# Kernel tuning notes

Measured on AMD Instinct MI355X. Metric: run time of the kernel, lower is better.

Reference implementation:

```python
import jax, jax.numpy as jnp
import numpy as np

B, T, C = 2, 2048, 1024
H = 16
HD = C // H  # head_size = 64
FF = 4 * C
EPS = 1e-5


def layernorm(x, g, b):
    mu = jnp.mean(x, axis=-1, keepdims=True)
    var = jnp.mean(jnp.square(x - mu), axis=-1, keepdims=True)
    return (x - mu) * jax.lax.rsqrt(var + EPS) * g + b


def setup_inputs() -> dict:
    key = jax.random.key(0)
    ks = jax.random.split(key, 12)
    s_c = 1.0 / np.sqrt(C)
    s_hc = 1.0 / np.sqrt(C)
    s_ff = 1.0 / np.sqrt(FF)
    return {
        "x": jax.random.normal(ks[0], (B, T, C), jnp.float32),
        "Wq": jax.random.normal(ks[1], (H, C, HD), jnp.float32) * s_hc,
        "Wk": jax.random.normal(ks[2], (H, C, HD), jnp.float32) * s_hc,
        "Wv": jax.random.normal(ks[3], (H, C, HD), jnp.float32) * s_hc,
        "Wo": jax.random.normal(ks[4], (C, C), jnp.float32) * s_c,
        "bo": jax.random.normal(ks[5], (C,), jnp.float32) * 0.01,
        "W1": jax.random.normal(ks[6], (C, FF), jnp.float32) * s_c,
        "b1": jax.random.normal(ks[7], (FF,), jnp.float32) * 0.01,
        "W2": jax.random.normal(ks[8], (FF, C), jnp.float32) * s_ff,
        "b2": jax.random.normal(ks[9], (C,), jnp.float32) * 0.01,
        "g1": jnp.ones((C,), jnp.float32),
        "be1": jnp.zeros((C,), jnp.float32),
        "g2": jnp.ones((C,), jnp.float32),
        "be2": jnp.zeros((C,), jnp.float32),
    }


def reference(x, Wq, Wk, Wv, Wo, bo, W1, b1, W2, b2, g1, be1, g2, be2):
    # --- self-attention sublayer (pre-LN, residual) ---
    h = layernorm(x, g1, be1)                               # [B,T,C]
    q = jnp.einsum("btc,hcd->bhtd", h, Wq)                   # [B,H,T,HD]
    k = jnp.einsum("btc,hcd->bhtd", h, Wk)
    v = jnp.einsum("btc,hcd->bhtd", h, Wv)
    scores = jnp.einsum("bhtd,bhsd->bhts", q, k) * (HD ** -0.5)
    causal = jnp.tril(jnp.ones((T, T), bool))
    scores = jnp.where(causal, scores, -jnp.inf)
    wei = jax.nn.softmax(scores, axis=-1)                    # [B,H,T,T]
    attn = jnp.einsum("bhts,bhsd->bhtd", wei, v)             # [B,H,T,HD]
    attn = attn.transpose(0, 2, 1, 3).reshape(B, T, H * HD)  # concat heads
    x = x + attn @ Wo + bo
    # --- feedforward sublayer (pre-LN, residual) ---
    h2 = layernorm(x, g2, be2)
    x = x + jax.nn.relu(h2 @ W1 + b1) @ W2 + b2
    return x
```

## Files before the change

### kernel.cpp

```cpp
#include <hip/hip_runtime.h>
#include <hip/hip_bf16.h>
#include <cstdint>
#include <cstddef>
#include <cstring>

#define B_ 2
#define T_ 2048
#define C_ 1024
#define H_ 16
#define HD_ 64
#define FF_ 4096
#define BT_ (B_*T_)

typedef __attribute__((ext_vector_type(8))) short short8;
typedef __attribute__((ext_vector_type(4))) float f32x4;

__device__ __forceinline__ float bf2f(ushort u) {
    return __uint_as_float(((uint)u) << 16);
}
__device__ __forceinline__ ushort f2bf(float f) {
    uint x = __float_as_uint(f);
    return (ushort)((x + 0x7fffu + ((x >> 16) & 1u)) >> 16);
}
__device__ __forceinline__ ushort f2bf_hw(float f) {
    __hip_bfloat16 h = __float2bfloat16(f);
    ushort u;
    __builtin_memcpy(&u, &h, 2);
    return u;
}

#define GLDS16(g, l)                                                        \
    __builtin_amdgcn_global_load_lds(                                       \
        (const __attribute__((address_space(1))) void*)(g),                 \
        (__attribute__((address_space(3))) void*)(l), 16, 0, 0)

__global__ __launch_bounds__(256) void ln_kernel(const float* __restrict__ x,
                                                 const float* __restrict__ g,
                                                 const float* __restrict__ b,
                                                 ushort* __restrict__ out) {
    int row = blockIdx.x;
    int tid = threadIdx.x;
    const float* xr = x + (size_t)row * C_;
    float4 v = *(const float4*)(xr + tid * 4);
    float s = v.x + v.y + v.z + v.w;
    float q = v.x*v.x + v.y*v.y + v.z*v.z + v.w*v.w;
    #pragma unroll
    for (int off = 32; off > 0; off >>= 1) {
        s += __shfl_down(s, off);
        q += __shfl_down(q, off);
    }
    __shared__ float ss[4], qs[4];
    if ((tid & 63) == 0) { ss[tid >> 6] = s; qs[tid >> 6] = q; }
    __syncthreads();
    s = ss[0] + ss[1] + ss[2] + ss[3];
    q = qs[0] + qs[1] + qs[2] + qs[3];
    float mu  = s * (1.0f / C_);
    float var = q * (1.0f / C_) - mu * mu;
    float r = rsqrtf(var + 1e-5f);
    float4 gv = *(const float4*)(g + tid * 4);
    float4 bv = *(const float4*)(b + tid * 4);
    ushort4 o;
    o.x = f2bf((v.x - mu) * r * gv.x + bv.x);
    o.y = f2bf((v.y - mu) * r * gv.y + bv.y);
    o.z = f2bf((v.z - mu) * r * gv.z + bv.z);
    o.w = f2bf((v.w - mu) * r * gv.w + bv.w);
    *(ushort4*)(out + (size_t)row * C_ + tid * 4) = o;
}

__global__ __launch_bounds__(256) void tcvt_kernel(const float* __restrict__ in,
                                                   ushort* __restrict__ out,
                                                   int R, int Cc, int ldo,
                                                   long in_bs, long out_bs) {
    __shared__ float tile[32][33];
    const float* inz = in + (size_t)blockIdx.z * in_bs;
    ushort* outz = out + (size_t)blockIdx.z * out_bs;
    int c0 = blockIdx.x * 32, r0 = blockIdx.y * 32;
    #pragma unroll
    for (int i = 0; i < 4; i++) {
        int r = threadIdx.y + i * 8;
        tile[r][threadIdx.x] = inz[(size_t)(r0 + r) * Cc + c0 + threadIdx.x];
    }
    __syncthreads();
    #pragma unroll
    for (int i = 0; i < 4; i++) {
        int c = threadIdx.y + i * 8;
        outz[(size_t)(c0 + c) * ldo + r0 + threadIdx.x] = f2bf(tile[threadIdx.x][c]);
    }
}

template<int EPI, bool OUT_BF16>
__global__ __launch_bounds__(512, 4) void gemm2(
    const ushort* __restrict__ A,
    const ushort* __restrict__ Bt,
    void* __restrict__ Cout,
    const float* __restrict__ bias,
    const float* __restrict__ resid,
    int M, int N, int K, int KS)
{
    __shared__ ushort As[2][128 * 32];
    __shared__ ushort Bs[2][256 * 32];

    int gx = gridDim.x;
    int nwg = gx * gridDim.y;
    int bid = blockIdx.y * gx + blockIdx.x;
    int cpx = nwg >> 3;
    int swz = (bid & 7) * cpx + (bid >> 3);
    int bx = swz % gx, by = swz / gx;

    int tid  = threadIdx.x;
    int lane = tid & 63;
    int lr = lane & 15, lq = lane >> 4;
    int wave = tid >> 6;
    int wr = wave >> 2, wc = wave & 3;
    int m0 = by * 128, n0 = bx * 256;
    int Koff = blockIdx.z * KS;
    size_t zoff = (size_t)blockIdx.z * ((size_t)M * N);

    f32x4 acc[4][4];
    #pragma unroll
    for (int i = 0; i < 4; i++)
        #pragma unroll
        for (int j = 0; j < 4; j++)
            acc[i][j] = {0.f, 0.f, 0.f, 0.f};

    int srow = tid >> 2;
    int scol = ((tid & 3) ^ ((srow >> 1) & 3)) * 8;
    const ushort* gA  = A  + (size_t)(m0 + srow) * K + Koff + scol;
    const ushort* gB0 = Bt + (size_t)(n0 + srow) * K + Koff + scol;
    const ushort* gB1 = Bt + (size_t)(n0 + 128 + srow) * K + Koff + scol;
    int NT = KS / 32;

    auto stage = [&](int kt, int buf) {
        int off = kt * 32;
        GLDS16(gA + off,  (char*)As[buf] + wave * 1024);
        GLDS16(gB0 + off, (char*)Bs[buf] + wave * 1024);
        GLDS16(gB1 + off, (char*)Bs[buf] + 8192 + wave * 1024);
    };

    stage(0, 0);
    stage(1, 1);
    asm volatile("s_waitcnt vmcnt(3)" ::: "memory");
    __builtin_amdgcn_s_barrier();

    int so = (lq ^ ((lr >> 1) & 3)) << 4;

    int cur = 0;
    for (int t = 0; t < NT; ++t) {
        const char* Ab = (const char*)As[cur] + (wr * 64 + lr) * 64 + so;
        const char* Bb = (const char*)Bs[cur] + (wc * 64 + lr) * 64 + so;

        short8 a[4], b[4];
        #pragma unroll
        for (int fr = 0; fr < 4; fr++)
            a[fr] = *(const short8*)(Ab + fr * 1024);
        #pragma unroll
        for (int fc = 0; fc < 4; fc++)
            b[fc] = *(const short8*)(Bb + fc * 1024);
        asm volatile("s_waitcnt lgkmcnt(0)" ::: "memory");
        __builtin_amdgcn_sched_barrier(0);
        __builtin_amdgcn_s_barrier();

        if (t + 2 < NT) stage(t + 2, cur);

        __builtin_amdgcn_s_setprio(1);
        #pragma unroll
        for (int fr = 0; fr < 4; fr++)
            #pragma unroll
            for (int fc = 0; fc < 4; fc++)
                acc[fr][fc] = __builtin_amdgcn_mfma_f32_16x16x32_bf16(
                    a[fr], b[fc], acc[fr][fc], 0, 0, 0);
        __builtin_amdgcn_s_setprio(0);

        if (t + 1 == NT) break;
        if (t + 2 < NT)
            asm volatile("s_waitcnt vmcnt(3)" ::: "memory");
        else
            asm volatile("s_waitcnt vmcnt(0)" ::: "memory");
        __builtin_amdgcn_s_barrier();
        cur ^= 1;
    }

    #pragma unroll
    for (int fr = 0; fr < 4; fr++) {
        #pragma unroll
        for (int fc = 0; fc < 4; fc++) {
            int col = n0 + wc * 64 + fc * 16 + lr;
            #pragma unroll
            for (int j = 0; j < 4; j++) {
                int row = m0 + wr * 64 + fr * 16 + lq * 4 + j;
                float v = acc[fr][fc][j];
                if (EPI & 1) v += bias[col];
                if (EPI & 2) v = fmaxf(v, 0.f);
                if (EPI & 4) v += resid[(size_t)row * N + col];
                if (OUT_BF16)
                    ((ushort*)Cout)[zoff + (size_t)row * N + col] = f2bf(v);
                else
                    ((float*)Cout)[zoff + (size_t)row * N + col] = v;
            }
        }
    }
}

__global__ __launch_bounds__(256) void vt_red(ushort* __restrict__ vt,
                                              const ushort* __restrict__ p) {
    size_t i = (size_t)blockIdx.x * 256 + threadIdx.x;
    ushort4 a = ((const ushort4*)p)[i];
    ushort4 b = ((const ushort4*)(p + (size_t)1024 * BT_))[i];
    ushort4 o;
    o.x = f2bf(bf2f(a.x) + bf2f(b.x));
    o.y = f2bf(bf2f(a.y) + bf2f(b.y));
    o.z = f2bf(bf2f(a.z) + bf2f(b.z));
    o.w = f2bf(bf2f(a.w) + bf2f(b.w));
    ((ushort4*)vt)[i] = o;
}

__global__ __launch_bounds__(256) void wo_ln(float* __restrict__ out,
                                             ushort* __restrict__ h,
                                             const ushort* __restrict__ p,
                                             const float* __restrict__ bo,
                                             const float* __restrict__ x,
                                             const float* __restrict__ g,
                                             const float* __restrict__ be) {
    int row = blockIdx.x;
    int tid = threadIdx.x;
    size_t base = (size_t)row * C_ + tid * 4;
    float4 v = *(const float4*)(x + base);
    float4 c = *(const float4*)(bo + tid * 4);
    #pragma unroll
    for (int z = 0; z < 4; z++) {
        ushort4 a = *(const ushort4*)(p + (size_t)z * BT_ * C_ + base);
        v.x += bf2f(a.x); v.y += bf2f(a.y);
        v.z += bf2f(a.z); v.w += bf2f(a.w);
    }
    v.x += c.x; v.y += c.y; v.z += c.z; v.w += c.w;
    *(float4*)(out + base) = v;

    float s = v.x + v.y + v.z + v.w;
    float q = v.x*v.x + v.y*v.y + v.z*v.z + v.w*v.w;
    #pragma unroll
    for (int off = 32; off > 0; off >>= 1) {
        s += __shfl_down(s, off);
        q += __shfl_down(q, off);
    }
    __shared__ float ss[4], qs[4];
    if ((tid & 63) == 0) { ss[tid >> 6] = s; qs[tid >> 6] = q; }
    __syncthreads();
    s = ss[0] + ss[1] + ss[2] + ss[3];
    q = qs[0] + qs[1] + qs[2] + qs[3];
    float mu  = s * (1.0f / C_);
    float var = q * (1.0f / C_) - mu * mu;
    float r = rsqrtf(var + 1e-5f);
    float4 gv = *(const float4*)(g + tid * 4);
    float4 bv = *(const float4*)(be + tid * 4);
    ushort4 o;
    o.x = f2bf((v.x - mu) * r * gv.x + bv.x);
    o.y = f2bf((v.y - mu) * r * gv.y + bv.y);
    o.z = f2bf((v.z - mu) * r * gv.z + bv.z);
    o.w = f2bf((v.w - mu) * r * gv.w + bv.w);
    *(ushort4*)(h + base) = o;
}

__global__ __launch_bounds__(256) void ff2_red4(float* __restrict__ out,
                                                const ushort* __restrict__ p,
                                                const float* __restrict__ b2) {
    size_t i = (size_t)blockIdx.x * 256 + threadIdx.x;
    float4 o = ((float4*)out)[i];
    float4 c = ((const float4*)b2)[i & 255];
    #pragma unroll
    for (int z = 0; z < 4; z++) {
        ushort4 a = ((const ushort4*)(p + (size_t)z * BT_ * C_))[i];
        o.x += bf2f(a.x); o.y += bf2f(a.y);
        o.z += bf2f(a.z); o.w += bf2f(a.w);
    }
    o.x += c.x; o.y += c.y; o.z += c.z; o.w += c.w;
    ((float4*)out)[i] = o;
}

__global__ __launch_bounds__(256, 3) void attn_mfma(const ushort* __restrict__ qk,
                                                    const ushort* __restrict__ vt,
                                                    ushort* __restrict__ Opart,
                                                    float* __restrict__ ml) {
    const float C2 = 0.18033688011f;
    const float THR2 = 12.0f;

    int flat = blockIdx.x;
    int xcd = flat & 7;
    int idx = flat >> 3;
    int bh  = xcd * 4 + (idx & 3);
    int qz  = idx >> 2;
    int qa  = 15 - (qz >> 1);
    int z   = qz & 1;

    int bb = bh >> 4;
    int head = bh & 15;
    int q0 = qa * 128;

    int tid  = threadIdx.x;
    int lane = tid & 63;
    int lr = lane & 15, lq = lane >> 4;
    int wave = tid >> 6;
    int qw = q0 + wave * 32;

    __shared__ ushort Ks[2][64 * 64];
    __shared__ ushort Vs[2][64 * 64];
    __shared__ ushort Ps[4][32 * 64];
    char* pw = (char*)Ps[wave];

    short8 qf[2][2];
    {
        const ushort* qb = qk + ((size_t)(bb * T_ + qw)) * 2048 + head * 64;
        #pragma unroll
        for (int mt = 0; mt < 2; mt++)
            #pragma unroll
            for (int kk = 0; kk < 2; kk++)
                qf[mt][kk] = *(const short8*)(qb + (size_t)(mt*16 + lr) * 2048 + kk*32 + lq*8);
    }

    f32x4 acc[2][4];
    f32x4 lsum[2];
    float m2[2][4];
    #pragma unroll
    for (int mt = 0; mt < 2; mt++) {
        #pragma unroll
        for (int dt = 0; dt < 4; dt++) acc[mt][dt] = {0.f, 0.f, 0.f, 0.f};
        lsum[mt] = {0.f, 0.f, 0.f, 0.f};
        #pragma unroll
        for (int j = 0; j < 4; j++) m2[mt][j] = -INFINITY;
    }

    const short8 onesf = {(short)0x3F80, (short)0x3F80, (short)0x3F80, (short)0x3F80,
                          (short)0x3F80, (short)0x3F80, (short)0x3F80, (short)0x3F80};

    int srow = tid >> 3;
    int ssc = ((tid & 7) ^ (srow & 7)) * 8;
    const ushort* kg0 = qk + ((size_t)(bb * T_ + srow)) * 2048 + 1024 + head * 64 + ssc;
    const ushort* vg0 = vt + ((size_t)(head * 64 + srow)) * 4096 + (size_t)bb * 2048 + ssc;

    auto stage = [&](int it, int buf) {
        int s0 = it * 64;
        char* Kb = (char*)Ks[buf] + wave * 1024;
        char* Vb = (char*)Vs[buf] + wave * 1024;
        GLDS16(kg0 + (size_t)s0 * 2048,        Kb);
        GLDS16(kg0 + (size_t)(s0 + 32) * 2048, Kb + 4096);
        GLDS16(vg0 + s0,                        Vb);
        GLDS16(vg0 + (size_t)32 * 4096 + s0,    Vb + 4096);
    };

    int nt = 2 * (qa + 1);
    stage(z, 0);
    __syncthreads();
    int cur = 0;

    for (int it = z; it < nt; it += 2) {
        if (it + 2 < nt) stage(it + 2, cur ^ 1);

        int s0h = it * 64;
        if (s0h <= qw + 31) {
            const ushort* Kc = Ks[cur];
            const ushort* Vc = Vs[cur];

            f32x4 sa[2][4];
            __builtin_amdgcn_s_setprio(1);
            #pragma unroll
            for (int n = 0; n < 4; n++) {
                int row = n*16 + lr;
                const char* kbase = (const char*)Kc + row*128;
                short8 kf0 = *(const short8*)(kbase + ((lq       ^ (row & 7)) << 4));
                short8 kf1 = *(const short8*)(kbase + (((4 + lq) ^ (row & 7)) << 4));
                #pragma unroll
                for (int mt = 0; mt < 2; mt++) {
                    f32x4 tq = {0.f, 0.f, 0.f, 0.f};
                    tq = __builtin_amdgcn_mfma_f32_16x16x32_bf16(qf[mt][0], kf0, tq, 0, 0, 0);
                    tq = __builtin_amdgcn_mfma_f32_16x16x32_bf16(qf[mt][1], kf1, tq, 0, 0, 0);
                    sa[mt][n] = tq;
                }
            }
            __builtin_amdgcn_s_setprio(0);

            if (s0h + 63 > qw) {
                #pragma unroll
                for (int mt = 0; mt < 2; mt++)
                    #pragma unroll
                    for (int n = 0; n < 4; n++)
                        #pragma unroll
                        for (int j = 0; j < 4; j++) {
                            int scolm = s0h + n*16 + lr;
                            int qrow = qw + mt*16 + lq*4 + j;
                            if (scolm > qrow) sa[mt][n][j] = -INFINITY;
                        }
            }

            float vmax2[2][4];
            bool growf = false;
            #pragma unroll
            for (int mt = 0; mt < 2; mt++) {
                #pragma unroll
                for (int j = 0; j < 4; j++) {
                    float v = fmaxf(fmaxf(sa[mt][0][j], sa[mt][1][j]),
                                    fmaxf(sa[mt][2][j], sa[mt][3][j]));
                    #pragma unroll
                    for (int off = 1; off < 16; off <<= 1)
                        v = fmaxf(v, __shfl_xor(v, off));
                    float v2 = v * C2;
                    vmax2[mt][j] = v2;
                    growf |= (v2 > m2[mt][j] + THR2);
                }
            }
            if (__any(growf)) {
                #pragma unroll
                for (int mt = 0; mt < 2; mt++)
                    #pragma unroll
                    for (int j = 0; j < 4; j++) {
                        float m2n = fmaxf(m2[mt][j], vmax2[mt][j]);
                        float corr = __builtin_amdgcn_exp2f(m2[mt][j] - m2n);
                        m2[mt][j] = m2n;
                        lsum[mt][j] *= corr;
                        #pragma unroll
                        for (int dt = 0; dt < 4; dt++)
                            acc[mt][dt][j] *= corr;
                    }
            }

            #pragma unroll
            for (int mt = 0; mt < 2; mt++)
                #pragma unroll
                for (int n = 0; n < 4; n++)
                    #pragma unroll
                    for (int j = 0; j < 4; j++) {
                        float p = __builtin_amdgcn_exp2f(
                            fmaf(sa[mt][n][j], C2, -m2[mt][j]));
                        int row = mt*16 + lq*4 + j;
                        int col = n*16 + lr;
                        int byte = row*128 + ((((col >> 3) ^ (row & 7))) << 4) + (col & 7)*2;
                        *(ushort*)(pw + byte) = f2bf_hw(p);
                    }

            short8 pf[2][2];
            #pragma unroll
            for (int mt = 0; mt < 2; mt++) {
                int row = mt*16 + lr;
                #pragma unroll
                for (int kk = 0; kk < 2; kk++)
                    pf[mt][kk] = *(const short8*)(pw + row*128
                                   + (((kk*4 + lq) ^ (row & 7)) << 4));
            }
            __builtin_amdgcn_s_setprio(1);
            #pragma unroll
            for (int kk = 0; kk < 2; kk++)
                #pragma unroll
                for (int mt = 0; mt < 2; mt++)
                    lsum[mt] = __builtin_amdgcn_mfma_f32_16x16x32_bf16(
                        pf[mt][kk], onesf, lsum[mt], 0, 0, 0);
            #pragma unroll
            for (int dt = 0; dt < 4; dt++) {
                int row = dt*16 + lr;
                const char* vbase = (const char*)Vc + row*128;
                #pragma unroll
                for (int kk = 0; kk < 2; kk++) {
                    short8 vf = *(const short8*)(vbase
                                  + (((kk*4 + lq) ^ (row & 7)) << 4));
                    #pragma unroll
                    for (int mt = 0; mt < 2; mt++)
                        acc[mt][dt] = __builtin_amdgcn_mfma_f32_16x16x32_bf16(
                            pf[mt][kk], vf, acc[mt][dt], 0, 0, 0);
                }
            }
            __builtin_amdgcn_s_setprio(0);
        }

        __syncthreads();
        cur ^= 1;
    }

    ushort* ob = Opart + (size_t)z * ((size_t)BT_ * C_)
               + ((size_t)(bb * T_ + qw)) * 1024 + head * 64;
    #pragma unroll
    for (int mt = 0; mt < 2; mt++)
        #pragma unroll
        for (int j = 0; j < 4; j++) {
            float l = lsum[mt][j];
            float inv = l > 0.f ? 1.0f / l : 0.f;
            #pragma unroll
            for (int dt = 0; dt < 4; dt++)
                ob[(size_t)(mt*16 + lq*4 + j) * 1024 + dt*16 + lr] =
                    f2bf(acc[mt][dt][j] * inv);
        }
    if (lr == 0) {
        float* mlz = ml + ((size_t)(z * 16 + head)) * (BT_ * 2);
        #pragma unroll
        for (int mt = 0; mt < 2; mt++)
            #pragma unroll
            for (int j = 0; j < 4; j++) {
                size_t row = (size_t)(bb * T_ + qw + mt*16 + lq*4 + j);
                *(float2*)(mlz + row * 2) = make_float2(m2[mt][j], lsum[mt][j]);
            }
    }
}

__global__ __launch_bounds__(256) void attn_comb(const ushort* __restrict__ Opart,
                                                 const float* __restrict__ ml,
                                                 ushort* __restrict__ outb) {
    int row = blockIdx.x;
    int tid = threadIdx.x;
    int col = tid * 4;
    int head = col >> 6;
    float2 ml0 = *(const float2*)(ml + ((size_t)head * BT_ + row) * 2);
    float2 ml1 = *(const float2*)(ml + ((size_t)(16 + head) * BT_ + row) * 2);
    float m = fmaxf(ml0.x, ml1.x);
    float w0 = ml0.y * __builtin_amdgcn_exp2f(ml0.x - m);
    float w1 = ml1.y * __builtin_amdgcn_exp2f(ml1.x - m);
    float inv = 1.0f / (w0 + w1);
    w0 *= inv; w1 *= inv;
    size_t idx = (size_t)row * C_ + col;
    ushort4 a = *(const ushort4*)(Opart + idx);
    ushort4 b = *(const ushort4*)(Opart + (size_t)BT_ * C_ + idx);
    ushort4 o;
    o.x = f2bf(bf2f(a.x) * w0 + bf2f(b.x) * w1);
    o.y = f2bf(bf2f(a.y) * w0 + bf2f(b.y) * w1);
    o.z = f2bf(bf2f(a.z) * w0 + bf2f(b.z) * w1);
    o.w = f2bf(bf2f(a.w) * w0 + bf2f(b.w) * w1);
    *(ushort4*)(outb + idx) = o;
}

extern "C" void kernel_launch(void* const* d_in, const int* in_sizes, int n_in,
                              void* d_out, int out_size, void* d_ws, size_t ws_size,
                              hipStream_t stream) {
    const float* x   = (const float*)d_in[0];
    const float* Wq  = (const float*)d_in[1];
    const float* Wk  = (const float*)d_in[2];
    const float* Wv  = (const float*)d_in[3];
    const float* Wo  = (const float*)d_in[4];
    const float* bo  = (const float*)d_in[5];
    const float* W1  = (const float*)d_in[6];
    const float* b1  = (const float*)d_in[7];
    const float* W2  = (const float*)d_in[8];
    const float* b2  = (const float*)d_in[9];
    const float* g1  = (const float*)d_in[10];
    const float* be1 = (const float*)d_in[11];
    const float* g2  = (const float*)d_in[12];
    const float* be2 = (const float*)d_in[13];
    float* out = (float*)d_out;

    char* ws = (char*)d_ws;
    const size_t MB = 1 << 20;
    ushort* h_bf    = (ushort*)(ws);
    ushort* qk_act  = (ushort*)(ws + 8*MB);
    ushort* vt      = (ushort*)(ws + 24*MB);
    ushort* attn_bf = (ushort*)(ws);
    ushort* W2_t    = (ushort*)(ws + 40*MB);
    ushort* qkvw    = (ushort*)(ws + 48*MB);
    ushort* Wo_t    = (ushort*)(ws + 54*MB);
    ushort* W1_t    = (ushort*)(ws + 56*MB);
    ushort* p_vt    = (ushort*)(ws + 64*MB);
    ushort* Opart   = (ushort*)(ws + 64*MB);
    float*  mlbuf   = (float*)(ws + 80*MB);
    ushort* p_wo    = (ushort*)(ws + 8*MB);
    ushort* ff1     = (ushort*)(ws + 8*MB);
    ushort* p_ff2   = (ushort*)(ws + 48*MB);

    const float* Wsrc[3] = {Wq, Wk, Wv};
    for (int w = 0; w < 3; w++) {
        tcvt_kernel<<<dim3(2, 32, 16), dim3(32, 8), 0, stream>>>(
            Wsrc[w], qkvw + (size_t)w * 1024 * 1024,
            1024, 64, 1024, 65536L, 65536L);
    }
    tcvt_kernel<<<dim3(32, 32, 1), dim3(32, 8), 0, stream>>>(
        Wo, Wo_t, 1024, 1024, 1024, 0L, 0L);
    tcvt_kernel<<<dim3(128, 32, 1), dim3(32, 8), 0, stream>>>(
        W1, W1_t, 1024, 4096, 1024, 0L, 0L);
    tcvt_kernel<<<dim3(32, 128, 1), dim3(32, 8), 0, stream>>>(
        W2, W2_t, 4096, 1024, 4096, 0L, 0L);

    ln_kernel<<<dim3(BT_), dim3(256), 0, stream>>>(x, g1, be1, h_bf);

    gemm2<0, true><<<dim3(2048/256, BT_/128, 1), dim3(512), 0, stream>>>(
        h_bf, qkvw, qk_act, nullptr, nullptr, BT_, 2048, C_, C_);
    gemm2<0, true><<<dim3(BT_/256, 1024/128, 2), dim3(512), 0, stream>>>(
        qkvw + (size_t)2*1024*1024, h_bf, p_vt, nullptr, nullptr, 1024, BT_, C_, 512);
    vt_red<<<dim3(1024*BT_/4/256), dim3(256), 0, stream>>>(vt, p_vt);

    attn_mfma<<<dim3(1024), dim3(256), 0, stream>>>(qk_act, vt, Opart, mlbuf);
    attn_comb<<<dim3(BT_), dim3(256), 0, stream>>>(Opart, mlbuf, attn_bf);

    gemm2<0, true><<<dim3(1024/256, BT_/128, 4), dim3(512), 0, stream>>>(
        attn_bf, Wo_t, p_wo, nullptr, nullptr, BT_, C_, C_, 256);
    wo_ln<<<dim3(BT_), dim3(256), 0, stream>>>(out, h_bf, p_wo, bo, x, g2, be2);

    gemm2<1|2, true><<<dim3(FF_/256, BT_/128, 1), dim3(512), 0, stream>>>(
        h_bf, W1_t, ff1, b1, nullptr, BT_, FF_, C_, C_);

    gemm2<0, true><<<dim3(1024/256, BT_/128, 4), dim3(512), 0, stream>>>(
        ff1, W2_t, p_ff2, nullptr, nullptr, BT_, C_, FF_, 1024);
    ff2_red4<<<dim3(BT_*C_/4/256), dim3(256), 0, stream>>>(out, p_ff2, b2);
}
```

Before: 259.3 us.

## Drop split-KV attention and combine pass; merge QKV weight conversions into one launch

```diff
diff --git a/kernel.cpp b/kernel.cpp
--- a/kernel.cpp
+++ b/kernel.cpp
@@ -88,6 +88,28 @@
     }
 }
 
+__global__ __launch_bounds__(256) void tcvt_qkv(const float* __restrict__ Wq,
+                                                const float* __restrict__ Wk,
+                                                const float* __restrict__ Wv,
+                                                ushort* __restrict__ qkvw) {
+    __shared__ float tile[32][33];
+    int z = blockIdx.z;
+    const float* in = (z < 16 ? Wq : (z < 32 ? Wk : Wv)) + (size_t)(z & 15) * 65536;
+    ushort* out = qkvw + (size_t)z * 65536;
+    int c0 = blockIdx.x * 32, r0 = blockIdx.y * 32;
+    #pragma unroll
+    for (int i = 0; i < 4; i++) {
+        int r = threadIdx.y + i * 8;
+        tile[r][threadIdx.x] = in[(size_t)(r0 + r) * 64 + c0 + threadIdx.x];
+    }
+    __syncthreads();
+    #pragma unroll
+    for (int i = 0; i < 4; i++) {
+        int c = threadIdx.y + i * 8;
+        out[(size_t)(c0 + c) * 1024 + r0 + threadIdx.x] = f2bf(tile[threadIdx.x][c]);
+    }
+}
+
 template<int EPI, bool OUT_BF16>
 __global__ __launch_bounds__(512, 4) void gemm2(
     const ushort* __restrict__ A,
@@ -278,8 +300,7 @@
 
 __global__ __launch_bounds__(256, 3) void attn_mfma(const ushort* __restrict__ qk,
                                                     const ushort* __restrict__ vt,
-                                                    ushort* __restrict__ Opart,
-                                                    float* __restrict__ ml) {
+                                                    ushort* __restrict__ outb) {
     const float C2 = 0.18033688011f;
     const float THR2 = 12.0f;
 
@@ -287,13 +308,11 @@
     int xcd = flat & 7;
     int idx = flat >> 3;
     int bh  = xcd * 4 + (idx & 3);
-    int qz  = idx >> 2;
-    int qa  = 15 - (qz >> 1);
-    int z   = qz & 1;
+    int qa  = 15 - (idx >> 2);
+    int q0 = qa * 128;
 
     int bb = bh >> 4;
     int head = bh & 15;
-    int q0 = qa * 128;
 
     int tid  = threadIdx.x;
     int lane = tid & 63;
@@ -347,12 +366,12 @@
     };
 
     int nt = 2 * (qa + 1);
-    stage(z, 0);
+    stage(0, 0);
     __syncthreads();
     int cur = 0;
 
-    for (int it = z; it < nt; it += 2) {
-        if (it + 2 < nt) stage(it + 2, cur ^ 1);
+    for (int it = 0; it < nt; it++) {
+        if (it + 1 < nt) stage(it + 1, cur ^ 1);
 
         int s0h = it * 64;
         if (s0h <= qw + 31) {
@@ -472,8 +491,7 @@
         cur ^= 1;
     }
 
-    ushort* ob = Opart + (size_t)z * ((size_t)BT_ * C_)
-               + ((size_t)(bb * T_ + qw)) * 1024 + head * 64;
+    ushort* ob = outb + ((size_t)(bb * T_ + qw)) * 1024 + head * 64;
     #pragma unroll
     for (int mt = 0; mt < 2; mt++)
         #pragma unroll
@@ -485,41 +503,6 @@
                 ob[(size_t)(mt*16 + lq*4 + j) * 1024 + dt*16 + lr] =
                     f2bf(acc[mt][dt][j] * inv);
         }
-    if (lr == 0) {
-        float* mlz = ml + ((size_t)(z * 16 + head)) * (BT_ * 2);
-        #pragma unroll
-        for (int mt = 0; mt < 2; mt++)
-            #pragma unroll
-            for (int j = 0; j < 4; j++) {
-                size_t row = (size_t)(bb * T_ + qw + mt*16 + lq*4 + j);
-                *(float2*)(mlz + row * 2) = make_float2(m2[mt][j], lsum[mt][j]);
-            }
-    }
-}
-
-__global__ __launch_bounds__(256) void attn_comb(const ushort* __restrict__ Opart,
-                                                 const float* __restrict__ ml,
-                                                 ushort* __restrict__ outb) {
-    int row = blockIdx.x;
-    int tid = threadIdx.x;
-    int col = tid * 4;
-    int head = col >> 6;
-    float2 ml0 = *(const float2*)(ml + ((size_t)head * BT_ + row) * 2);
-    float2 ml1 = *(const float2*)(ml + ((size_t)(16 + head) * BT_ + row) * 2);
-    float m = fmaxf(ml0.x, ml1.x);
-    float w0 = ml0.y * __builtin_amdgcn_exp2f(ml0.x - m);
-    float w1 = ml1.y * __builtin_amdgcn_exp2f(ml1.x - m);
-    float inv = 1.0f / (w0 + w1);
-    w0 *= inv; w1 *= inv;
-    size_t idx = (size_t)row * C_ + col;
-    ushort4 a = *(const ushort4*)(Opart + idx);
-    ushort4 b = *(const ushort4*)(Opart + (size_t)BT_ * C_ + idx);
-    ushort4 o;
-    o.x = f2bf(bf2f(a.x) * w0 + bf2f(b.x) * w1);
-    o.y = f2bf(bf2f(a.y) * w0 + bf2f(b.y) * w1);
-    o.z = f2bf(bf2f(a.z) * w0 + bf2f(b.z) * w1);
-    o.w = f2bf(bf2f(a.w) * w0 + bf2f(b.w) * w1);
-    *(ushort4*)(outb + idx) = o;
 }
 
 extern "C" void kernel_launch(void* const* d_in, const int* in_sizes, int n_in,
@@ -552,18 +535,11 @@
     ushort* Wo_t    = (ushort*)(ws + 54*MB);
     ushort* W1_t    = (ushort*)(ws + 56*MB);
     ushort* p_vt    = (ushort*)(ws + 64*MB);
-    ushort* Opart   = (ushort*)(ws + 64*MB);
-    float*  mlbuf   = (float*)(ws + 80*MB);
     ushort* p_wo    = (ushort*)(ws + 8*MB);
     ushort* ff1     = (ushort*)(ws + 8*MB);
     ushort* p_ff2   = (ushort*)(ws + 48*MB);
 
-    const float* Wsrc[3] = {Wq, Wk, Wv};
-    for (int w = 0; w < 3; w++) {
-        tcvt_kernel<<<dim3(2, 32, 16), dim3(32, 8), 0, stream>>>(
-            Wsrc[w], qkvw + (size_t)w * 1024 * 1024,
-            1024, 64, 1024, 65536L, 65536L);
-    }
+    tcvt_qkv<<<dim3(2, 32, 48), dim3(32, 8), 0, stream>>>(Wq, Wk, Wv, qkvw);
     tcvt_kernel<<<dim3(32, 32, 1), dim3(32, 8), 0, stream>>>(
         Wo, Wo_t, 1024, 1024, 1024, 0L, 0L);
     tcvt_kernel<<<dim3(128, 32, 1), dim3(32, 8), 0, stream>>>(
@@ -579,8 +555,7 @@
         qkvw + (size_t)2*1024*1024, h_bf, p_vt, nullptr, nullptr, 1024, BT_, C_, 512);
     vt_red<<<dim3(1024*BT_/4/256), dim3(256), 0, stream>>>(vt, p_vt);
 
-    attn_mfma<<<dim3(1024), dim3(256), 0, stream>>>(qk_act, vt, Opart, mlbuf);
-    attn_comb<<<dim3(BT_), dim3(256), 0, stream>>>(Opart, mlbuf, attn_bf);
+    attn_mfma<<<dim3(512), dim3(256), 0, stream>>>(qk_act, vt, attn_bf);
 
     gemm2<0, true><<<dim3(1024/256, BT_/128, 4), dim3(512), 0, stream>>>(
         attn_bf, Wo_t, p_wo, nullptr, nullptr, BT_, C_, C_, 256);
```

Measured after the change: 282.2 us. 1.09x slower.
